# Kernel optimization log

Hardware: AMD Instinct MI355X
Metric: run time of the kernel (lower is better)

The kernel has to match this reference:

```python
import math
import jax, jax.numpy as jnp
import numpy as np

B, S, HID = 2, 2048, 3072
NH, HD = 32, 96            # num_heads, head_dim; num_kv_heads == num_heads (n_rep = 1)
OP = NH * HD + 2 * (NH * HD)  # 9216


def _rope_tables(seq_len, head_dim, theta=10000.0):
    inv_freq = 1.0 / (theta ** (np.arange(0, head_dim, 2, dtype=np.float32) / head_dim))
    t = np.arange(seq_len, dtype=np.float32)
    freqs = np.outer(t, inv_freq)                      # [S, HD/2]
    emb = np.concatenate([freqs, freqs], axis=-1)      # [S, HD]
    return jnp.asarray(np.cos(emb)), jnp.asarray(np.sin(emb))


def setup_inputs() -> dict:
    key = jax.random.key(0)
    k1, k2, k3 = jax.random.split(key, 3)
    hidden_states = jax.random.normal(k1, (B, S, HID), dtype=jnp.float32)
    cos, sin = _rope_tables(S, HD)
    # additive causal mask [B, 1, S, S]
    neg = jnp.finfo(jnp.float32).min
    causal = jnp.where(jnp.tril(jnp.ones((S, S), dtype=bool)), 0.0, neg)
    attention_mask = jnp.broadcast_to(causal[None, None], (B, 1, S, S)).astype(jnp.float32)
    Wqkv = jax.random.normal(k2, (HID, OP), dtype=jnp.float32) * (HID ** -0.5)
    Wo = jax.random.normal(k3, (NH * HD, HID), dtype=jnp.float32) * ((NH * HD) ** -0.5)
    return {"hidden_states": hidden_states, "cos": cos, "sin": sin,
            "attention_mask": attention_mask, "Wqkv": Wqkv, "Wo": Wo}


def _rotate_half(x):
    x1, x2 = jnp.split(x, 2, axis=-1)
    return jnp.concatenate([-x2, x1], axis=-1)


def reference(hidden_states, cos, sin, attention_mask, Wqkv, Wo):
    bsz, q_len, _ = hidden_states.shape
    qkv = hidden_states @ Wqkv                                    # [B,S,OP]
    q, k, v = jnp.split(qkv, [NH * HD, 2 * NH * HD], axis=-1)
    # [B,S,H*D] -> [B,H,S,D]
    to_bhsd = lambda t: t.reshape(bsz, q_len, NH, HD).transpose(0, 2, 1, 3)
    q, k, v = to_bhsd(q), to_bhsd(k), to_bhsd(v)
    c = cos[None, None]                                           # [1,1,S,D]
    s = sin[None, None]
    q = q * c + _rotate_half(q) * s
    k = k * c + _rotate_half(k) * s
    # num_key_value_groups == 1, so repeat_kv is identity.
    scores = jnp.einsum('bhqd,bhkd->bhqk', q, k) / math.sqrt(HD)  # [B,H,S,S]
    scores = scores + attention_mask
    attn = jax.nn.softmax(scores.astype(jnp.float32), axis=-1).astype(v.dtype)
    # dropout p=0.0 / eval -> identity
    out = jnp.einsum('bhqk,bhkd->bhqd', attn, v)                  # [B,H,S,D]
    out = out.transpose(0, 2, 1, 3).reshape(bsz, q_len, NH * HD)
    return out @ Wo                                               # [B,S,HID]
```

## Files before the change

### kernel.cpp

```cpp
#include <hip/hip_runtime.h>

typedef __bf16  bf16x8 __attribute__((ext_vector_type(8)));
typedef float   f32x4  __attribute__((ext_vector_type(4)));
typedef short   i16x8  __attribute__((ext_vector_type(8)));
typedef unsigned short u16x4 __attribute__((ext_vector_type(4)));

__device__ __forceinline__ float bf2f(unsigned short u) {
    union { unsigned int i; float f; } v; v.i = ((unsigned int)u) << 16; return v.f;
}
__device__ __forceinline__ unsigned short f2bf(float f) {
    union { float f; unsigned int i; } v; v.f = f;
    unsigned int r = v.i + 0x7FFFu + ((v.i >> 16) & 1u);
    return (unsigned short)(r >> 16);
}
__device__ __forceinline__ void gload_lds16(const void* g, void* l) {
    __builtin_amdgcn_global_load_lds(
        (const __attribute__((address_space(1))) void*)g,
        (__attribute__((address_space(3))) void*)l, 16, 0, 0);
}

__global__ __launch_bounds__(256) void cast_f32_bf16(
    const float* __restrict__ in, unsigned short* __restrict__ out, int n8)
{
    int i = blockIdx.x * 256 + threadIdx.x;
    if (i >= n8) return;
    const f32x4* p = (const f32x4*)(in + (long)i * 8);
    f32x4 a = p[0], b = p[1];
    i16x8 o;
    o[0]=(short)f2bf(a[0]); o[1]=(short)f2bf(a[1]); o[2]=(short)f2bf(a[2]); o[3]=(short)f2bf(a[3]);
    o[4]=(short)f2bf(b[0]); o[5]=(short)f2bf(b[1]); o[6]=(short)f2bf(b[2]); o[7]=(short)f2bf(b[3]);
    *(i16x8*)(out + (long)i * 8) = o;
}

__global__ __launch_bounds__(256) void transpose_cast(
    const float* __restrict__ in, unsigned short* __restrict__ out, int R, int C)
{
    __shared__ float tile[64][65];
    int c0 = blockIdx.x * 64, r0 = blockIdx.y * 64;
    int tx = threadIdx.x & 63, ty = threadIdx.x >> 6;
#pragma unroll
    for (int i = 0; i < 64; i += 4)
        tile[ty + i][tx] = in[(long)(r0 + ty + i) * C + c0 + tx];
    __syncthreads();
#pragma unroll
    for (int i = 0; i < 64; i += 4)
        out[(long)(c0 + ty + i) * R + r0 + tx] = f2bf(tile[tx][ty + i]);
}

template <int MODE>
__global__ __launch_bounds__(512, 2) void gemm256(
    const unsigned short* __restrict__ A, const unsigned short* __restrict__ B,
    int K, int N, int nbx,
    unsigned short* __restrict__ Qo, unsigned short* __restrict__ Ko,
    unsigned short* __restrict__ Vo, float* __restrict__ Cf)
{
    __shared__ __align__(16) unsigned short As[2][256 * 64];
    __shared__ __align__(16) unsigned short Bs[2][256 * 64];
    const int t = threadIdx.x;
    const int w = t >> 6, l = t & 63, lhi = (l >> 4), llo = l & 15;
    const int wm = w >> 2, wn = w & 3;

    const int nwg = gridDim.x, cpx = nwg >> 3;
    const int wg = ((int)blockIdx.x & 7) * cpx + ((int)blockIdx.x >> 3);
    const int bx = wg % nbx, by = wg / nbx;
    const int m0 = bx << 8, n0 = by << 8;

    const unsigned short* aG[4];
    const unsigned short* bG[4];
    int ldsOff[4];
#pragma unroll
    for (int i = 0; i < 4; ++i) {
        int j = i * 512 + t;
        int row = j >> 3;
        int c = (j & 7) ^ (row & 7);
        aG[i] = A + (long)(m0 + row) * K + c * 8;
        bG[i] = B + (long)(n0 + row) * K + c * 8;
        ldsOff[i] = (i * 512 + (w << 6)) * 8;
    }

    const int nkt = K >> 6;
#pragma unroll
    for (int i = 0; i < 4; ++i) {
        gload_lds16(aG[i], &As[0][ldsOff[i]]);
        gload_lds16(bG[i], &Bs[0][ldsOff[i]]);
    }
#pragma unroll
    for (int i = 0; i < 4; ++i) {
        gload_lds16(aG[i] + 64, &As[1][ldsOff[i]]);
        gload_lds16(bG[i] + 64, &Bs[1][ldsOff[i]]);
    }

    f32x4 acc[8][4] = {};

    for (int kt = 0; kt < nkt; ++kt) {
        const int c = kt & 1;
        if (kt < nkt - 1) asm volatile("s_waitcnt vmcnt(8)" ::: "memory");
        else              asm volatile("s_waitcnt vmcnt(0)" ::: "memory");
        __builtin_amdgcn_s_barrier();

        const unsigned short* Ab = As[c];
        const unsigned short* Bb = Bs[c];
        bf16x8 af[8];
#pragma unroll
        for (int kh = 0; kh < 2; ++kh) {
#pragma unroll
            for (int mi = 0; mi < 8; ++mi) {
                int row = (wm << 7) + (mi << 4) + llo;
                int cc = ((kh << 2) + lhi) ^ (row & 7);
                af[mi] = __builtin_bit_cast(bf16x8, *(const i16x8*)&Ab[row * 64 + cc * 8]);
            }
#pragma unroll
            for (int nh = 0; nh < 2; ++nh) {
                bf16x8 b0, b1;
                {
                    int row = (wn << 6) + (nh << 5) + llo;
                    int cc = ((kh << 2) + lhi) ^ (row & 7);
                    b0 = __builtin_bit_cast(bf16x8, *(const i16x8*)&Bb[row * 64 + cc * 8]);
                    row += 16;
                    cc = ((kh << 2) + lhi) ^ (row & 7);
                    b1 = __builtin_bit_cast(bf16x8, *(const i16x8*)&Bb[row * 64 + cc * 8]);
                }
                const bool last = (kh == 1) && (nh == 1);
                if (last) {
                    asm volatile("s_waitcnt lgkmcnt(0)" ::: "memory");
                }
                __builtin_amdgcn_s_barrier();
                if (last && (kt + 2 < nkt)) {
                    const long off = (long)(kt + 2) * 64;
#pragma unroll
                    for (int i = 0; i < 4; ++i) {
                        gload_lds16(aG[i] + off, &As[c][ldsOff[i]]);
                        gload_lds16(bG[i] + off, &Bs[c][ldsOff[i]]);
                    }
                }
                __builtin_amdgcn_s_setprio(1);
#pragma unroll
                for (int mi = 0; mi < 8; ++mi) {
                    acc[mi][(nh << 1)]     = __builtin_amdgcn_mfma_f32_16x16x32_bf16(
                        af[mi], b0, acc[mi][(nh << 1)], 0, 0, 0);
                    acc[mi][(nh << 1) + 1] = __builtin_amdgcn_mfma_f32_16x16x32_bf16(
                        af[mi], b1, acc[mi][(nh << 1) + 1], 0, 0, 0);
                }
                __builtin_amdgcn_s_setprio(0);
            }
        }
    }

#pragma unroll
    for (int mi = 0; mi < 8; ++mi) {
        int s0g = m0 + (wm << 7) + (mi << 4) + (lhi << 2);
#pragma unroll
        for (int ni = 0; ni < 4; ++ni) {
            int gcol = n0 + (wn << 6) + (ni << 4) + llo;
            if (MODE == 1) {
#pragma unroll
                for (int r = 0; r < 4; ++r)
                    Cf[(long)(s0g + r) * N + gcol] = acc[mi][ni][r];
            } else {
                int seg = gcol / 3072;
                int cc2 = gcol - seg * 3072;
                int h = cc2 / 96, d = cc2 - h * 96;
                int b = s0g >> 11, s = s0g & 2047;
                long bh = (long)((b << 5) + h);
                if (seg == 2) {
                    u16x4 pv;
#pragma unroll
                    for (int r = 0; r < 4; ++r) pv[r] = f2bf(acc[mi][ni][r]);
                    *(u16x4*)(Vo + (bh * 96 + d) * 2048 + s) = pv;
                } else {
                    unsigned short* dst = seg ? Ko : Qo;
#pragma unroll
                    for (int r = 0; r < 4; ++r)
                        dst[(bh * 2048 + s + r) * 96 + d] = f2bf(acc[mi][ni][r]);
                }
            }
        }
    }
}

__global__ __launch_bounds__(256) void rope_kernel(
    unsigned short* __restrict__ Qb, unsigned short* __restrict__ Kb,
    const float* __restrict__ cosT, const float* __restrict__ sinT)
{
    int i = blockIdx.x * 256 + threadIdx.x;
    int d6 = i % 6;
    int sbh = i / 6;
    int s = sbh & 2047;
    long base = (long)sbh * 96 + d6 * 8;
    const f32x4* cp = (const f32x4*)(cosT + s * 96 + d6 * 8);
    const f32x4* sp = (const f32x4*)(sinT + s * 96 + d6 * 8);
    f32x4 c0 = cp[0], c1 = cp[1], s0 = sp[0], s1 = sp[1];
    float cv[8] = {c0[0],c0[1],c0[2],c0[3],c1[0],c1[1],c1[2],c1[3]};
    float sv[8] = {s0[0],s0[1],s0[2],s0[3],s1[0],s1[1],s1[2],s1[3]};
    i16x8 qlo = *(i16x8*)(Qb + base), qhi = *(i16x8*)(Qb + base + 48);
    i16x8 klo = *(i16x8*)(Kb + base), khi = *(i16x8*)(Kb + base + 48);
    i16x8 qlo2, qhi2, klo2, khi2;
#pragma unroll
    for (int j = 0; j < 8; ++j) {
        float ql = bf2f((unsigned short)qlo[j]), qh = bf2f((unsigned short)qhi[j]);
        float kl = bf2f((unsigned short)klo[j]), kh = bf2f((unsigned short)khi[j]);
        qlo2[j] = (short)f2bf(ql * cv[j] - qh * sv[j]);
        qhi2[j] = (short)f2bf(qh * cv[j] + ql * sv[j]);
        klo2[j] = (short)f2bf(kl * cv[j] - kh * sv[j]);
        khi2[j] = (short)f2bf(kh * cv[j] + kl * sv[j]);
    }
    *(i16x8*)(Qb + base) = qlo2; *(i16x8*)(Qb + base + 48) = qhi2;
    *(i16x8*)(Kb + base) = klo2; *(i16x8*)(Kb + base + 48) = khi2;
}

__global__ __launch_bounds__(256, 3) void attn_fwd(
    const unsigned short* __restrict__ Q, const unsigned short* __restrict__ Kt,
    const unsigned short* __restrict__ Vg, unsigned short* __restrict__ O)
{
    __shared__ unsigned short Kl[64 * 104];
    __shared__ unsigned short Vl[96 * 72];
    __shared__ unsigned short Pl[4][16 * 88];
    const int t = threadIdx.x;
    const int w = t >> 6, l = t & 63, lhi = l >> 4, llo = l & 15;
    const int bx = blockIdx.x, bh = blockIdx.y;
    constexpr float C2 = 0.14724450f;

    int klds[3], vlds[3];
    const unsigned short* kg[3];
    const unsigned short* vg[3];
#pragma unroll
    for (int i = 0; i < 3; ++i) {
        int c = t + i * 256;
        int srow = c / 12, scc = c % 12;
        kg[i] = Kt + ((long)bh * 2048 + srow) * 96 + scc * 8;
        klds[i] = srow * 104 + scc * 8;
        int vrow = c >> 3, vch = c & 7;
        vg[i] = Vg + ((long)bh * 96 + vrow) * 2048 + vch * 8;
        vlds[i] = vrow * 72 + vch * 8;
    }

    const int b = bh >> 5, h = bh & 31;

    for (int pass = 0; pass < 2; ++pass) {
        const int qb = pass ? (31 - bx) : bx;
        const int q0 = qb << 6;

        bf16x8 qf[3];
        {
            const unsigned short* qp =
                Q + ((long)bh * 2048 + q0 + (w << 4) + llo) * 96 + (lhi << 3);
#pragma unroll
            for (int kf = 0; kf < 3; ++kf)
                qf[kf] = __builtin_bit_cast(bf16x8, *(const i16x8*)(qp + kf * 32));
        }

        f32x4 oacc[6] = {};
        float m_r[4] = {-1e30f, -1e30f, -1e30f, -1e30f};
        float l_l[4] = {0.f, 0.f, 0.f, 0.f};

        i16x8 kreg[3], vreg[3];
#pragma unroll
        for (int i = 0; i < 3; ++i) {
            kreg[i] = *(const i16x8*)kg[i];
            vreg[i] = *(const i16x8*)vg[i];
        }

        for (int kt = 0; kt <= qb; ++kt) {
            __syncthreads();
#pragma unroll
            for (int i = 0; i < 3; ++i) {
                *(i16x8*)&Kl[klds[i]] = kreg[i];
                *(i16x8*)&Vl[vlds[i]] = vreg[i];
            }
            __syncthreads();
            if (kt < qb) {
#pragma unroll
                for (int i = 0; i < 3; ++i) {
                    kreg[i] = *(const i16x8*)(kg[i] + (long)(kt + 1) * 64 * 96);
                    vreg[i] = *(const i16x8*)(vg[i] + (kt + 1) * 64);
                }
            }

            f32x4 sa[4] = {};
#pragma unroll
            for (int kf = 0; kf < 3; ++kf) {
#pragma unroll
                for (int nf = 0; nf < 4; ++nf) {
                    bf16x8 bfr = __builtin_bit_cast(bf16x8,
                        *(const i16x8*)&Kl[(nf * 16 + llo) * 104 + kf * 32 + (lhi << 3)]);
                    sa[nf] = __builtin_amdgcn_mfma_f32_16x16x32_bf16(qf[kf], bfr, sa[nf], 0, 0, 0);
                }
            }
            if (kt == qb) {
#pragma unroll
                for (int nf = 0; nf < 4; ++nf) {
                    int col = nf * 16 + llo;
#pragma unroll
                    for (int r = 0; r < 4; ++r)
                        if (col > (w << 4) + (lhi << 2) + r) sa[nf][r] = -1e30f;
                }
            }

#pragma unroll
            for (int r = 0; r < 4; ++r) {
                float mx = fmaxf(fmaxf(sa[0][r], sa[1][r]), fmaxf(sa[2][r], sa[3][r]));
                mx = fmaxf(mx, __shfl_xor(mx, 1));
                mx = fmaxf(mx, __shfl_xor(mx, 2));
                mx = fmaxf(mx, __shfl_xor(mx, 4));
                mx = fmaxf(mx, __shfl_xor(mx, 8));
                if (__any(mx > m_r[r] + 54.0f)) {
                    float mnew = fmaxf(m_r[r], mx);
                    float scl = exp2f((m_r[r] - mnew) * C2);
                    l_l[r] *= scl;
#pragma unroll
                    for (int nf = 0; nf < 6; ++nf) oacc[nf][r] *= scl;
                    m_r[r] = mnew;
                }
                float mC = m_r[r] * C2;
                float rs = 0.f;
#pragma unroll
                for (int nf = 0; nf < 4; ++nf) {
                    float p = exp2f(fmaf(sa[nf][r], C2, -mC));
                    rs += p;
                    Pl[w][((lhi << 2) + r) * 88 + nf * 16 + llo] = f2bf(p);
                }
                l_l[r] += rs;
            }

#pragma unroll
            for (int kf = 0; kf < 2; ++kf) {
                bf16x8 pa = __builtin_bit_cast(bf16x8,
                    *(const i16x8*)&Pl[w][llo * 88 + kf * 32 + (lhi << 3)]);
#pragma unroll
                for (int nf = 0; nf < 6; ++nf) {
                    bf16x8 bv = __builtin_bit_cast(bf16x8,
                        *(const i16x8*)&Vl[(nf * 16 + llo) * 72 + kf * 32 + (lhi << 3)]);
                    oacc[nf] = __builtin_amdgcn_mfma_f32_16x16x32_bf16(pa, bv, oacc[nf], 0, 0, 0);
                }
            }
        }

#pragma unroll
        for (int r = 0; r < 4; ++r) {
            float s = l_l[r];
            s += __shfl_xor(s, 1);
            s += __shfl_xor(s, 2);
            s += __shfl_xor(s, 4);
            s += __shfl_xor(s, 8);
            float inv = 1.0f / s;
            long ob = ((long)(b * 2048 + q0 + (w << 4) + (lhi << 2) + r)) * 3072 + h * 96;
#pragma unroll
            for (int nf = 0; nf < 6; ++nf)
                O[ob + nf * 16 + llo] = f2bf(oacc[nf][r] * inv);
        }
    }
}

extern "C" void kernel_launch(void* const* d_in, const int* in_sizes, int n_in,
                              void* d_out, int out_size, void* d_ws, size_t ws_size,
                              hipStream_t stream) {
    const float* hidden = (const float*)d_in[0];
    const float* cosT   = (const float*)d_in[1];
    const float* sinT   = (const float*)d_in[2];
    const float* Wqkv   = (const float*)d_in[4];
    const float* Wo     = (const float*)d_in[5];
    float* out = (float*)d_out;

    char* ws = (char*)d_ws;
    unsigned short* Ah  = (unsigned short*)ws;
    unsigned short* WqT = (unsigned short*)(ws + 25165824);
    unsigned short* Qb  = (unsigned short*)(ws + 25165824 + 56623104);
    unsigned short* Kb  = Qb + 12582912;
    unsigned short* Vb  = Kb + 12582912;

    cast_f32_bf16<<<6144, 256, 0, stream>>>(hidden, Ah, 1572864);
    transpose_cast<<<dim3(144, 48), 256, 0, stream>>>(Wqkv, WqT, 3072, 9216);
    gemm256<0><<<576, 512, 0, stream>>>(Ah, WqT, 3072, 9216, 16, Qb, Kb, Vb, nullptr);
    transpose_cast<<<dim3(48, 48), 256, 0, stream>>>(Wo, WqT, 3072, 3072);
    rope_kernel<<<3072, 256, 0, stream>>>(Qb, Kb, cosT, sinT);
    attn_fwd<<<dim3(16, 64), 256, 0, stream>>>(Qb, Kb, Vb, Ah);
    gemm256<1><<<192, 512, 0, stream>>>(Ah, WqT, 3072, 3072, 16,
                                        nullptr, nullptr, nullptr, out);
}
```

Measured before the change: 598.5 us.

## Restructure GEMM main loop into 8-phase quarter-tile pipelined schedule

The 256x256 bf16 GEMM main loop now splits each 64-wide K tile into four quarter-tile sub-phases (A/B halves). Global-to-LDS loads for the next tiles are issued one half-tile at a time, interleaved with the MFMA work on the current buffer, with explicit vmcnt waits at phase boundaries. The intent is to overlap memory traffic with compute more evenly and reduce stalls at the per-tile barrier. In exchange it adds more barriers per K tile and depends on a subtle buffer-reuse schedule. It also assumes the number of K tiles is even.

```diff
diff --git a/kernel.cpp b/kernel.cpp
--- a/kernel.cpp
+++ b/kernel.cpp
@@ -57,7 +57,7 @@
     __shared__ __align__(16) unsigned short As[2][256 * 64];
     __shared__ __align__(16) unsigned short Bs[2][256 * 64];
     const int t = threadIdx.x;
-    const int w = t >> 6, l = t & 63, lhi = (l >> 4), llo = l & 15;
+    const int w = t >> 6, l = t & 63, lhi = l >> 4, llo = l & 15;
     const int wm = w >> 2, wn = w & 3;
 
     const int nwg = gridDim.x, cpx = nwg >> 3;
@@ -65,93 +65,114 @@
     const int bx = wg % nbx, by = wg / nbx;
     const int m0 = bx << 8, n0 = by << 8;
 
-    const unsigned short* aG[4];
-    const unsigned short* bG[4];
-    int ldsOff[4];
-#pragma unroll
-    for (int i = 0; i < 4; ++i) {
-        int j = i * 512 + t;
-        int row = j >> 3;
-        int c = (j & 7) ^ (row & 7);
-        aG[i] = A + (long)(m0 + row) * K + c * 8;
-        bG[i] = B + (long)(n0 + row) * K + c * 8;
-        ldsOff[i] = (i * 512 + (w << 6)) * 8;
-    }
-
-    const int nkt = K >> 6;
-#pragma unroll
-    for (int i = 0; i < 4; ++i) {
-        gload_lds16(aG[i], &As[0][ldsOff[i]]);
-        gload_lds16(bG[i], &Bs[0][ldsOff[i]]);
-    }
-#pragma unroll
-    for (int i = 0; i < 4; ++i) {
-        gload_lds16(aG[i] + 64, &As[1][ldsOff[i]]);
-        gload_lds16(bG[i] + 64, &Bs[1][ldsOff[i]]);
-    }
+    const int swzc = ((l & 7) ^ (l >> 3)) << 3;
+    const unsigned short* aS = A + (long)(m0 + w * 8 + (l >> 3)) * K + swzc;
+    const int bRow0 = ((w >> 2) << 6) + ((w & 3) << 3) + (l >> 3);
+    const unsigned short* bS = B + (long)(n0 + bRow0) * K + swzc;
+
+    const int nkt = K >> 6, niter = nkt >> 1;
+
+#define STAGE_A(buf, mh, kt)                                                    \
+    {                                                                           \
+        _Pragma("unroll")                                                       \
+        for (int i_ = 0; i_ < 2; ++i_) {                                        \
+            int ro_ = i_ * 128 + (mh) * 64;                                     \
+            gload_lds16(aS + (long)ro_ * K + (kt) * 64,                         \
+                        &As[buf][(ro_ + w * 8) * 64]);                          \
+        }                                                                       \
+    }
+#define STAGE_B(buf, nh, kt)                                                    \
+    {                                                                           \
+        _Pragma("unroll")                                                       \
+        for (int i_ = 0; i_ < 2; ++i_) {                                        \
+            int lr_ = ((i_ * 2 + (w >> 2)) << 6) + ((nh) << 5) + ((w & 3) << 3);\
+            gload_lds16(bS + (long)(i_ * 128 + (nh) * 32) * K + (kt) * 64,      \
+                        &Bs[buf][lr_ * 64]);                                    \
+        }                                                                       \
+    }
+
+    STAGE_A(0, 0, 0); STAGE_B(0, 0, 0); STAGE_A(0, 1, 0); STAGE_B(0, 1, 0);
+    STAGE_A(1, 0, 1); STAGE_B(1, 0, 1);
+    asm volatile("s_waitcnt vmcnt(0)" ::: "memory");
+    __builtin_amdgcn_s_barrier();
 
     f32x4 acc[8][4] = {};
 
-    for (int kt = 0; kt < nkt; ++kt) {
-        const int c = kt & 1;
-        if (kt < nkt - 1) asm volatile("s_waitcnt vmcnt(8)" ::: "memory");
-        else              asm volatile("s_waitcnt vmcnt(0)" ::: "memory");
-        __builtin_amdgcn_s_barrier();
-
-        const unsigned short* Ab = As[c];
-        const unsigned short* Bb = Bs[c];
-        bf16x8 af[8];
-#pragma unroll
-        for (int kh = 0; kh < 2; ++kh) {
-#pragma unroll
-            for (int mi = 0; mi < 8; ++mi) {
-                int row = (wm << 7) + (mi << 4) + llo;
-                int cc = ((kh << 2) + lhi) ^ (row & 7);
-                af[mi] = __builtin_bit_cast(bf16x8, *(const i16x8*)&Ab[row * 64 + cc * 8]);
-            }
-#pragma unroll
-            for (int nh = 0; nh < 2; ++nh) {
-                bf16x8 b0, b1;
-                {
-                    int row = (wn << 6) + (nh << 5) + llo;
-                    int cc = ((kh << 2) + lhi) ^ (row & 7);
-                    b0 = __builtin_bit_cast(bf16x8, *(const i16x8*)&Bb[row * 64 + cc * 8]);
-                    row += 16;
-                    cc = ((kh << 2) + lhi) ^ (row & 7);
-                    b1 = __builtin_bit_cast(bf16x8, *(const i16x8*)&Bb[row * 64 + cc * 8]);
-                }
-                const bool last = (kh == 1) && (nh == 1);
-                if (last) {
-                    asm volatile("s_waitcnt lgkmcnt(0)" ::: "memory");
-                }
-                __builtin_amdgcn_s_barrier();
-                if (last && (kt + 2 < nkt)) {
-                    const long off = (long)(kt + 2) * 64;
-#pragma unroll
-                    for (int i = 0; i < 4; ++i) {
-                        gload_lds16(aG[i] + off, &As[c][ldsOff[i]]);
-                        gload_lds16(bG[i] + off, &Bs[c][ldsOff[i]]);
-                    }
-                }
-                __builtin_amdgcn_s_setprio(1);
-#pragma unroll
-                for (int mi = 0; mi < 8; ++mi) {
-                    acc[mi][(nh << 1)]     = __builtin_amdgcn_mfma_f32_16x16x32_bf16(
-                        af[mi], b0, acc[mi][(nh << 1)], 0, 0, 0);
-                    acc[mi][(nh << 1) + 1] = __builtin_amdgcn_mfma_f32_16x16x32_bf16(
-                        af[mi], b1, acc[mi][(nh << 1) + 1], 0, 0, 0);
-                }
-                __builtin_amdgcn_s_setprio(0);
-            }
-        }
-    }
+    for (int it = 0; it < niter; ++it) {
+        const int kt0 = it << 1;
+        const bool lastIt = (it == niter - 1);
+#pragma unroll
+        for (int p = 0; p < 8; ++p) {
+            const int mh = (p >> 1) & 1, nh = p & 1, bsel = p >> 2;
+            const unsigned short* Ab = As[bsel];
+            const unsigned short* Bb = Bs[bsel];
+
+            bf16x8 af[4][2], bfv[2][2];
+#pragma unroll
+            for (int mi = 0; mi < 4; ++mi) {
+                int row = (wm << 7) + (mh << 6) + (mi << 4) + llo;
+#pragma unroll
+                for (int kk = 0; kk < 2; ++kk) {
+                    int cc = ((kk << 2) + lhi) ^ (row & 7);
+                    af[mi][kk] = __builtin_bit_cast(bf16x8,
+                        *(const i16x8*)&Ab[row * 64 + cc * 8]);
+                }
+            }
+#pragma unroll
+            for (int ni = 0; ni < 2; ++ni) {
+                int row = (wn << 6) + (nh << 5) + (ni << 4) + llo;
+#pragma unroll
+                for (int kk = 0; kk < 2; ++kk) {
+                    int cc = ((kk << 2) + lhi) ^ (row & 7);
+                    bfv[ni][kk] = __builtin_bit_cast(bf16x8,
+                        *(const i16x8*)&Bb[row * 64 + cc * 8]);
+                }
+            }
+
+            {
+                const int toff = (p < 2) ? 1 : ((p >= 6) ? 3 : 2);
+                const int st = kt0 + toff;
+                if (st < nkt) {
+                    const int sreg = 1 - ((p >> 1) & 1);
+                    const int sbuf = (p < 2 || p >= 6) ? 1 : 0;
+                    if ((p & 1) == 0) STAGE_A(sbuf, sreg, st)
+                    else              STAGE_B(sbuf, sreg, st)
+                }
+            }
+
+            __builtin_amdgcn_s_barrier();
+            __builtin_amdgcn_s_setprio(1);
+#pragma unroll
+            for (int kk = 0; kk < 2; ++kk)
+#pragma unroll
+                for (int mi = 0; mi < 4; ++mi)
+#pragma unroll
+                    for (int ni = 0; ni < 2; ++ni)
+                        acc[(mh << 2) + mi][(nh << 1) + ni] =
+                            __builtin_amdgcn_mfma_f32_16x16x32_bf16(
+                                af[mi][kk], bfv[ni][kk],
+                                acc[(mh << 2) + mi][(nh << 1) + ni], 0, 0, 0);
+            __builtin_amdgcn_s_setprio(0);
+            asm volatile("s_waitcnt lgkmcnt(0)" ::: "memory");
+            __builtin_amdgcn_sched_barrier(0);
+            if (p == 3) {
+                if (lastIt) asm volatile("s_waitcnt vmcnt(0)" ::: "memory");
+                else        asm volatile("s_waitcnt vmcnt(4)" ::: "memory");
+            } else if (p == 7) {
+                if (!lastIt) asm volatile("s_waitcnt vmcnt(4)" ::: "memory");
+            }
+            __builtin_amdgcn_s_barrier();
+        }
+    }
+#undef STAGE_A
+#undef STAGE_B
 
 #pragma unroll
     for (int mi = 0; mi < 8; ++mi) {
-        int s0g = m0 + (wm << 7) + (mi << 4) + (lhi << 2);
+        int s0g = m0 + (wm << 7) + ((mi >> 2) << 6) + ((mi & 3) << 4) + (lhi << 2);
 #pragma unroll
         for (int ni = 0; ni < 4; ++ni) {
-            int gcol = n0 + (wn << 6) + (ni << 4) + llo;
+            int gcol = n0 + (wn << 6) + ((ni >> 1) << 5) + ((ni & 1) << 4) + llo;
             if (MODE == 1) {
 #pragma unroll
                 for (int r = 0; r < 4; ++r)
```

Measured after the change: 591.0 us. About the same (-1.3%).
